# Kernel tuning notes

Hardware: AMD Instinct MI355X
Metric: run time of the kernel (lower is better)

## Reference

```python
import jax, jax.numpy as jnp
import numpy as np

NEG = -9e15  # matches torch's -9000000000000000.0 masking constant


def setup_inputs() -> dict:
    key = jax.random.key(0)
    kq, kk, kv, ka = jax.random.split(key, 4)
    B, H, N, d = 8, 8, 1024, 128
    queries = jax.random.normal(kq, (B, H, N, d), dtype=jnp.float32)
    keys = jax.random.normal(kk, (B, H, N, d), dtype=jnp.float32)
    values = jax.random.normal(kv, (B, H, N, d), dtype=jnp.float32)
    adj = jax.random.randint(ka, (N, N), 0, 2, dtype=jnp.int32)
    return {"queries": queries, "keys": keys, "values": values, "adj": adj}


def reference(queries, keys, values, adj):
    # scores: [B,H,N,N]; original divides by the constant 8 (not sqrt(dim))
    e = jnp.einsum("bhnd,bhmd->bhnm", queries, keys) / 8.0
    # adjacency mask [N,N] broadcasts over batch and heads
    att = jnp.where(adj > 0, e, jnp.asarray(NEG, e.dtype))
    att = jax.nn.softmax(att, axis=-1)
    # dropout is identity in eval mode
    h = jnp.einsum("bhnm,bhmd->bhnd", att, values)  # [B,H,N,d]
    B, H, N, d = h.shape
    # original uses .view (raw reshape), NOT a permute
    return jnp.reshape(h, (N, B, H, d))
```

## Files before the change

kernel.cpp:

```cpp
#include <hip/hip_runtime.h>
#include <hip/hip_bf16.h>


typedef __bf16 bf16x8 __attribute__((ext_vector_type(8)));
typedef float  f32x4  __attribute__((ext_vector_type(4)));
typedef unsigned int u32;

#define NSEQ 1024
#define DH   128
#define BN   64
#define NKT  16
#define TILE_ELEMS (BN * DH)
#define C1 0.1803368801111244f
#define C2 11.5415603271110070f

__device__ __forceinline__ float f4get(const float4& v, int c) {
    return (c == 0) ? v.x : (c == 1) ? v.y : (c == 2) ? v.z : v.w;
}

__device__ __forceinline__ void gload_lds16(const void* g, void* l) {
    __builtin_amdgcn_global_load_lds(
        (const __attribute__((address_space(1))) u32*)g,
        (__attribute__((address_space(3))) u32*)l, 16, 0, 0);
}

__global__ __launch_bounds__(256)
void prepack_kernel(const float* __restrict__ K, const float* __restrict__ V,
                    __bf16* __restrict__ Kws, __bf16* __restrict__ Vws)
{
    const int tid = threadIdx.x;
    const int id  = blockIdx.x;
    const size_t gbase = (size_t)(id >> 4) * NSEQ * DH + (size_t)(id & 15) * BN * DH;
    __bf16* ko = Kws + (size_t)id * TILE_ELEMS;
    __bf16* vo = Vws + (size_t)id * TILE_ELEMS;

    {
        const int r  = tid >> 2;
        const int c0 = (tid & 3) * 4;
        #pragma unroll
        for (int cc = 0; cc < 4; ++cc) {
            const int c = c0 + cc;
            const float* src = K + gbase + (size_t)r * DH + c * 8;
            float4 a = *(const float4*)src;
            float4 b = *(const float4*)(src + 4);
            bf16x8 w;
            w[0]=(__bf16)a.x; w[1]=(__bf16)a.y; w[2]=(__bf16)a.z; w[3]=(__bf16)a.w;
            w[4]=(__bf16)b.x; w[5]=(__bf16)b.y; w[6]=(__bf16)b.z; w[7]=(__bf16)b.w;
            const int cs = (c & 8) | ((c ^ (r & 7)) & 7);
            *(bf16x8*)(ko + r * DH + cs * 8) = w;
        }
    }
    {
        const int vkvb = tid >> 5;
        const int vdb  = tid & 31;
        float4 vr[8];
        #pragma unroll
        for (int rr = 0; rr < 8; ++rr)
            vr[rr] = *(const float4*)(V + gbase + (size_t)(vkvb * 8 + rr) * DH + vdb * 4);
        #pragma unroll
        for (int c = 0; c < 4; ++c) {
            const int d = vdb * 4 + c;
            bf16x8 w;
            #pragma unroll
            for (int j = 0; j < 8; ++j) w[j] = (__bf16)f4get(vr[j], c);
            const int cs = vkvb ^ (d & 7);
            *(bf16x8*)(vo + d * BN + cs * 8) = w;
        }
    }
}

__global__ __launch_bounds__(256, 2)
void attn_fast(const float* __restrict__ Q, const __bf16* __restrict__ Kws,
               const __bf16* __restrict__ Vws, const int* __restrict__ adj,
               float* __restrict__ out)
{
    __shared__ __attribute__((aligned(16))) __bf16 Kt[TILE_ELEMS];
    __shared__ __attribute__((aligned(16))) __bf16 Vt[TILE_ELEMS];
    __shared__ __attribute__((aligned(16))) __bf16 Ps[128 * 72];

    const int tid  = threadIdx.x;
    const int wave = tid >> 6;
    const int lane = tid & 63;
    const int n16  = lane & 15;
    const int quad = lane >> 4;
    const int m7   = n16 & 7;

    const int id = blockIdx.x;
    const int bh = (id & 7) * 8 + ((id >> 3) & 7);
    const int q0 = (id >> 6) * 128;
    const size_t base  = (size_t)bh * NSEQ * DH;
    const size_t tile0 = (size_t)(bh * NKT) * TILE_ELEMS;

    bf16x8 qf[2][4];
    #pragma unroll
    for (int rt = 0; rt < 2; ++rt)
        #pragma unroll
        for (int ks = 0; ks < 4; ++ks) {
            const float* src = Q + base + (size_t)(q0 + wave * 32 + rt * 16 + n16) * DH
                             + ks * 32 + quad * 8;
            float4 a = *(const float4*)src;
            float4 b = *(const float4*)(src + 4);
            bf16x8 w;
            w[0]=(__bf16)a.x; w[1]=(__bf16)a.y; w[2]=(__bf16)a.z; w[3]=(__bf16)a.w;
            w[4]=(__bf16)b.x; w[5]=(__bf16)b.y; w[6]=(__bf16)b.z; w[7]=(__bf16)b.w;
            qf[rt][ks] = w;
        }

    f32x4 o[2][8];
    #pragma unroll
    for (int rt = 0; rt < 2; ++rt)
        #pragma unroll
        for (int i = 0; i < 8; ++i) o[rt][i] = (f32x4){0.f, 0.f, 0.f, 0.f};
    float lp[2][4] = {{0.f,0.f,0.f,0.f},{0.f,0.f,0.f,0.f}};

    for (int kt = 0; kt < NKT; ++kt) {
        const int kv0 = kt * BN;
        __syncthreads();

        const __bf16* ktile = Kws + tile0 + (size_t)kt * TILE_ELEMS;
        const __bf16* vtile = Vws + tile0 + (size_t)kt * TILE_ELEMS;
        #pragma unroll
        for (int j = 0; j < 4; ++j) {
            const int off = wave * 2048 + j * 512;
            gload_lds16(ktile + off + lane * 8, &Kt[off]);
            gload_lds16(vtile + off + lane * 8, &Vt[off]);
        }
        __syncthreads();

        int am[2][4][4];
        #pragma unroll
        for (int rt = 0; rt < 2; ++rt)
            #pragma unroll
            for (int i = 0; i < 4; ++i)
                #pragma unroll
                for (int t = 0; t < 4; ++t)
                    am[rt][i][t] = adj[(size_t)(q0 + wave * 32 + rt * 16 + quad * 4 + i) * NSEQ
                                       + kv0 + t * 16 + n16];

        float sc[2][4][4];
        #pragma unroll
        for (int t = 0; t < 4; ++t) {
            f32x4 acc0 = (f32x4){0.f, 0.f, 0.f, 0.f};
            f32x4 acc1 = (f32x4){0.f, 0.f, 0.f, 0.f};
            #pragma unroll
            for (int ks = 0; ks < 4; ++ks) {
                const int c  = ks * 4 + quad;
                const int cs = (c & 8) | ((c ^ m7) & 7);
                bf16x8 bfr = *(const bf16x8*)(&Kt[(t * 16 + n16) * DH + cs * 8]);
                acc0 = __builtin_amdgcn_mfma_f32_16x16x32_bf16(qf[0][ks], bfr, acc0, 0, 0, 0);
                acc1 = __builtin_amdgcn_mfma_f32_16x16x32_bf16(qf[1][ks], bfr, acc1, 0, 0, 0);
            }
            #pragma unroll
            for (int i = 0; i < 4; ++i) { sc[0][t][i] = acc0[i]; sc[1][t][i] = acc1[i]; }
        }

        #pragma unroll
        for (int rt = 0; rt < 2; ++rt)
            #pragma unroll
            for (int i = 0; i < 4; ++i) {
                const int prow = wave * 32 + rt * 16 + quad * 4 + i;
                float rowsum = 0.f;
                #pragma unroll
                for (int t = 0; t < 4; ++t) {
                    float p = exp2f(sc[rt][t][i] * C1 - C2);
                    p = (am[rt][i][t] > 0) ? p : 0.f;
                    rowsum += p;
                    Ps[prow * 72 + t * 16 + n16] = (__bf16)p;
                }
                lp[rt][i] += rowsum;
            }

        #pragma unroll
        for (int ks = 0; ks < 2; ++ks) {
            bf16x8 pf0 = *(const bf16x8*)(&Ps[(wave * 32 + n16)      * 72 + ks * 32 + quad * 8]);
            bf16x8 pf1 = *(const bf16x8*)(&Ps[(wave * 32 + 16 + n16) * 72 + ks * 32 + quad * 8]);
            #pragma unroll
            for (int nt = 0; nt < 8; ++nt) {
                const int d  = nt * 16 + n16;
                const int cs = (ks * 4 + quad) ^ m7;
                bf16x8 vf = *(const bf16x8*)(&Vt[d * BN + cs * 8]);
                o[0][nt] = __builtin_amdgcn_mfma_f32_16x16x32_bf16(pf0, vf, o[0][nt], 0, 0, 0);
                o[1][nt] = __builtin_amdgcn_mfma_f32_16x16x32_bf16(pf1, vf, o[1][nt], 0, 0, 0);
            }
        }
    }

    #pragma unroll
    for (int rt = 0; rt < 2; ++rt) {
        float linv[4];
        #pragma unroll
        for (int i = 0; i < 4; ++i) {
            float ls = lp[rt][i];
            ls += __shfl_xor(ls, 1);
            ls += __shfl_xor(ls, 2);
            ls += __shfl_xor(ls, 4);
            ls += __shfl_xor(ls, 8);
            linv[i] = 1.0f / fmaxf(ls, 1e-30f);
        }
        const int qrow = q0 + wave * 32 + rt * 16 + quad * 4;
        #pragma unroll
        for (int nt = 0; nt < 8; ++nt)
            #pragma unroll
            for (int i = 0; i < 4; ++i)
                out[base + (size_t)(qrow + i) * DH + nt * 16 + n16] = o[rt][nt][i] * linv[i];
    }
}

#define KS_STRIDE 136
#define VT_STRIDE 64
#define PS_STRIDE 72

__global__ __launch_bounds__(256, 4)
void attn_fallback(const float* __restrict__ Q, const float* __restrict__ K,
                   const float* __restrict__ V, const int* __restrict__ adj,
                   float* __restrict__ out)
{
    __shared__ __attribute__((aligned(16))) __bf16 KsP[BN * KS_STRIDE];
    __shared__ __attribute__((aligned(16))) __bf16 Vts[DH * VT_STRIDE];
    const int tid = threadIdx.x;
    const int wave = tid >> 6, lane = tid & 63, n16 = lane & 15, quad = lane >> 4;
    const int id = blockIdx.x;
    const int bh = (id & 7) * 8 + ((id >> 3) & 7);
    const int q0 = (id >> 6) * 64;
    const size_t base = (size_t)bh * NSEQ * DH;
    const int rp = tid >> 4, kcol = (tid & 15) * 8, db = tid & 31, kvb = tid >> 5;
    bf16x8 qf[4];
    #pragma unroll
    for (int ks = 0; ks < 4; ++ks) {
        const float* src = Q + base + (size_t)(q0 + wave * 16 + n16) * DH + ks * 32 + quad * 8;
        float4 a = *(const float4*)src; float4 b = *(const float4*)(src + 4);
        bf16x8 w;
        w[0]=(__bf16)a.x; w[1]=(__bf16)a.y; w[2]=(__bf16)a.z; w[3]=(__bf16)a.w;
        w[4]=(__bf16)b.x; w[5]=(__bf16)b.y; w[6]=(__bf16)b.z; w[7]=(__bf16)b.w;
        qf[ks] = w;
    }
    f32x4 o[8];
    #pragma unroll
    for (int i = 0; i < 8; ++i) o[i] = (f32x4){0.f, 0.f, 0.f, 0.f};
    float lp[4] = {0.f, 0.f, 0.f, 0.f};
    const int qrow = q0 + wave * 16 + quad * 4;
    for (int kt = 0; kt < NKT; ++kt) {
        const int kv0 = kt * BN;
        __syncthreads();
        #pragma unroll
        for (int it = 0; it < 4; ++it) {
            int row = 16 * it + rp;
            const float* src = K + base + (size_t)(kv0 + row) * DH + kcol;
            float4 a = *(const float4*)src; float4 b = *(const float4*)(src + 4);
            bf16x8 w;
            w[0]=(__bf16)a.x; w[1]=(__bf16)a.y; w[2]=(__bf16)a.z; w[3]=(__bf16)a.w;
            w[4]=(__bf16)b.x; w[5]=(__bf16)b.y; w[6]=(__bf16)b.z; w[7]=(__bf16)b.w;
            *(bf16x8*)(&KsP[row * KS_STRIDE + kcol]) = w;
        }
        {
            float4 vreg[8];
            #pragma unroll
            for (int rr = 0; rr < 8; ++rr)
                vreg[rr] = *(const float4*)(V + base + (size_t)(kv0 + kvb * 8 + rr) * DH + db * 4);
            #pragma unroll
            for (int c = 0; c < 4; ++c) {
                bf16x8 w;
                #pragma unroll
                for (int j = 0; j < 8; ++j) w[j] = (__bf16)f4get(vreg[j], c);
                int d = db * 4 + c, s = (d ^ (d >> 3)) & 7;
                *(bf16x8*)(&Vts[d * VT_STRIDE + ((kvb ^ s) << 3)]) = w;
            }
        }
        __syncthreads();
        int am[4][4];
        #pragma unroll
        for (int i = 0; i < 4; ++i)
            #pragma unroll
            for (int t = 0; t < 4; ++t)
                am[i][t] = adj[(size_t)(qrow + i) * NSEQ + kv0 + t * 16 + n16];
        float sc[4][4];
        #pragma unroll
        for (int t = 0; t < 4; ++t) {
            f32x4 acc = (f32x4){0.f, 0.f, 0.f, 0.f};
            #pragma unroll
            for (int ks = 0; ks < 4; ++ks) {
                bf16x8 bfr = *(const bf16x8*)(&KsP[(t * 16 + n16) * KS_STRIDE + ks * 32 + quad * 8]);
                acc = __builtin_amdgcn_mfma_f32_16x16x32_bf16(qf[ks], bfr, acc, 0, 0, 0);
            }
            #pragma unroll
            for (int i = 0; i < 4; ++i) sc[t][i] = acc[i];
        }
        __syncthreads();
        #pragma unroll
        for (int i = 0; i < 4; ++i) {
            const int prow = wave * 16 + quad * 4 + i;
            float rowsum = 0.f;
            #pragma unroll
            for (int t = 0; t < 4; ++t) {
                float p = exp2f(sc[t][i] * C1 - C2);
                p = (am[i][t] > 0) ? p : 0.f;
                rowsum += p;
                KsP[prow * PS_STRIDE + t * 16 + n16] = (__bf16)p;
            }
            lp[i] += rowsum;
        }
        #pragma unroll
        for (int ks = 0; ks < 2; ++ks) {
            bf16x8 pf = *(const bf16x8*)(&KsP[(wave * 16 + n16) * PS_STRIDE + ks * 32 + quad * 8]);
            #pragma unroll
            for (int nt = 0; nt < 8; ++nt) {
                int d = nt * 16 + n16, s = (d ^ (d >> 3)) & 7, kvbr = ks * 4 + quad;
                bf16x8 vf = *(const bf16x8*)(&Vts[d * VT_STRIDE + ((kvbr ^ s) << 3)]);
                o[nt] = __builtin_amdgcn_mfma_f32_16x16x32_bf16(pf, vf, o[nt], 0, 0, 0);
            }
        }
    }
    float linv[4];
    #pragma unroll
    for (int i = 0; i < 4; ++i) {
        float ls = lp[i];
        ls += __shfl_xor(ls, 1); ls += __shfl_xor(ls, 2);
        ls += __shfl_xor(ls, 4); ls += __shfl_xor(ls, 8);
        linv[i] = 1.0f / fmaxf(ls, 1e-30f);
    }
    #pragma unroll
    for (int nt = 0; nt < 8; ++nt)
        #pragma unroll
        for (int i = 0; i < 4; ++i)
            out[base + (size_t)(qrow + i) * DH + nt * 16 + n16] = o[nt][i] * linv[i];
}

extern "C" void kernel_launch(void* const* d_in, const int* in_sizes, int n_in,
                              void* d_out, int out_size, void* d_ws, size_t ws_size,
                              hipStream_t stream) {
    const float* Q   = (const float*)d_in[0];
    const float* K   = (const float*)d_in[1];
    const float* V   = (const float*)d_in[2];
    const int*   adj = (const int*)d_in[3];
    float* out = (float*)d_out;
    const size_t need = (size_t)2 * 64 * NKT * TILE_ELEMS * sizeof(__bf16);
    if (ws_size >= need) {
        __bf16* Kws = (__bf16*)d_ws;
        __bf16* Vws = Kws + (size_t)64 * NKT * TILE_ELEMS;
        prepack_kernel<<<1024, 256, 0, stream>>>(K, V, Kws, Vws);
        attn_fast<<<512, 256, 0, stream>>>(Q, Kws, Vws, adj, out);
    } else {
        attn_fallback<<<1024, 256, 0, stream>>>(Q, K, V, adj, out);
    }
}
```

Before: 194.6 us.

## Double-buffer K tiles and overlap V/K LDS loads with QK compute

Gives K a second LDS buffer and prefetches the next K tile while the current one is used. The V load is issued before the QK MFMA so it overlaps with the score compute. Synchronisation moves to hand-placed s_waitcnt/s_barrier with scheduling barriers, and s_setprio raises priority around the MFMA sections. This hides global-to-LDS latency that the two __syncthreads per tile used to expose, at the cost of more LDS and fragile vmcnt counting (vmcnt(4) assumes exactly the K prefetch loads are outstanding). The last iteration also prefetches a tile that wraps around and is never used.

```diff
diff --git a/kernel.cpp b/kernel.cpp
--- a/kernel.cpp
+++ b/kernel.cpp
@@ -74,7 +74,7 @@
                const __bf16* __restrict__ Vws, const int* __restrict__ adj,
                float* __restrict__ out)
 {
-    __shared__ __attribute__((aligned(16))) __bf16 Kt[TILE_ELEMS];
+    __shared__ __attribute__((aligned(16))) __bf16 Kt[2][TILE_ELEMS];
     __shared__ __attribute__((aligned(16))) __bf16 Vt[TILE_ELEMS];
     __shared__ __attribute__((aligned(16))) __bf16 Ps[128 * 72];
 
@@ -113,19 +113,20 @@
         for (int i = 0; i < 8; ++i) o[rt][i] = (f32x4){0.f, 0.f, 0.f, 0.f};
     float lp[2][4] = {{0.f,0.f,0.f,0.f},{0.f,0.f,0.f,0.f}};
 
+    #pragma unroll
+    for (int j = 0; j < 4; ++j) {
+        const int off = wave * 2048 + j * 512;
+        gload_lds16(Kws + tile0 + off + lane * 8, &Kt[0][off]);
+    }
+
     for (int kt = 0; kt < NKT; ++kt) {
         const int kv0 = kt * BN;
-        __syncthreads();
-
-        const __bf16* ktile = Kws + tile0 + (size_t)kt * TILE_ELEMS;
-        const __bf16* vtile = Vws + tile0 + (size_t)kt * TILE_ELEMS;
-        #pragma unroll
-        for (int j = 0; j < 4; ++j) {
-            const int off = wave * 2048 + j * 512;
-            gload_lds16(ktile + off + lane * 8, &Kt[off]);
-            gload_lds16(vtile + off + lane * 8, &Vt[off]);
-        }
-        __syncthreads();
+
+        __builtin_amdgcn_sched_barrier(0);
+        asm volatile("s_waitcnt vmcnt(0)" ::: "memory");
+        __builtin_amdgcn_sched_barrier(0);
+        __builtin_amdgcn_s_barrier();
+        __builtin_amdgcn_sched_barrier(0);
 
         int am[2][4][4];
         #pragma unroll
@@ -136,8 +137,33 @@
                 for (int t = 0; t < 4; ++t)
                     am[rt][i][t] = adj[(size_t)(q0 + wave * 32 + rt * 16 + quad * 4 + i) * NSEQ
                                        + kv0 + t * 16 + n16];
-
+        __builtin_amdgcn_sched_barrier(0);
+
+        {
+            const __bf16* vtile = Vws + tile0 + (size_t)kt * TILE_ELEMS;
+            #pragma unroll
+            for (int j = 0; j < 4; ++j) {
+                const int off = wave * 2048 + j * 512;
+                gload_lds16(vtile + off + lane * 8, &Vt[off]);
+            }
+        }
+        __builtin_amdgcn_sched_barrier(0);
+
+        {
+            const int ktn = (kt + 1) & (NKT - 1);
+            const __bf16* ktile = Kws + tile0 + (size_t)ktn * TILE_ELEMS;
+            __bf16* kdst = &Kt[ktn & 1][0];
+            #pragma unroll
+            for (int j = 0; j < 4; ++j) {
+                const int off = wave * 2048 + j * 512;
+                gload_lds16(ktile + off + lane * 8, kdst + off);
+            }
+        }
+        __builtin_amdgcn_sched_barrier(0);
+
+        const __bf16* Kc = &Kt[kt & 1][0];
         float sc[2][4][4];
+        __builtin_amdgcn_s_setprio(1);
         #pragma unroll
         for (int t = 0; t < 4; ++t) {
             f32x4 acc0 = (f32x4){0.f, 0.f, 0.f, 0.f};
@@ -146,13 +172,14 @@
             for (int ks = 0; ks < 4; ++ks) {
                 const int c  = ks * 4 + quad;
                 const int cs = (c & 8) | ((c ^ m7) & 7);
-                bf16x8 bfr = *(const bf16x8*)(&Kt[(t * 16 + n16) * DH + cs * 8]);
+                bf16x8 bfr = *(const bf16x8*)(Kc + (t * 16 + n16) * DH + cs * 8);
                 acc0 = __builtin_amdgcn_mfma_f32_16x16x32_bf16(qf[0][ks], bfr, acc0, 0, 0, 0);
                 acc1 = __builtin_amdgcn_mfma_f32_16x16x32_bf16(qf[1][ks], bfr, acc1, 0, 0, 0);
             }
             #pragma unroll
             for (int i = 0; i < 4; ++i) { sc[0][t][i] = acc0[i]; sc[1][t][i] = acc1[i]; }
         }
+        __builtin_amdgcn_s_setprio(0);
 
         #pragma unroll
         for (int rt = 0; rt < 2; ++rt)
@@ -170,6 +197,13 @@
                 lp[rt][i] += rowsum;
             }
 
+        __builtin_amdgcn_sched_barrier(0);
+        asm volatile("s_waitcnt vmcnt(4) lgkmcnt(0)" ::: "memory");
+        __builtin_amdgcn_sched_barrier(0);
+        __builtin_amdgcn_s_barrier();
+        __builtin_amdgcn_sched_barrier(0);
+
+        __builtin_amdgcn_s_setprio(1);
         #pragma unroll
         for (int ks = 0; ks < 2; ++ks) {
             bf16x8 pf0 = *(const bf16x8*)(&Ps[(wave * 32 + n16)      * 72 + ks * 32 + quad * 8]);
@@ -183,6 +217,7 @@
                 o[1][nt] = __builtin_amdgcn_mfma_f32_16x16x32_bf16(pf1, vf, o[1][nt], 0, 0, 0);
             }
         }
+        __builtin_amdgcn_s_setprio(0);
     }
 
     #pragma unroll
```

Result: slower. 199.7 us (+2.6%).
